# Optimization experiments

Measured on AMD Instinct MI355X. Metric: run time of the kernel, lower is better.

## Reference

```python
import jax, jax.numpy as jnp
import numpy as np

NUM_SEGMENTS = 10000
B, S, D = 4, 200000, 64

def setup_inputs() -> dict:
    key = jax.random.key(0)
    k1, k2, k3 = jax.random.split(key, 3)
    data = jax.random.normal(k1, (B, S, D), dtype=jnp.float32)
    v = jax.random.normal(k2, (B, S, D), dtype=jnp.float32)
    segment_index = jax.random.randint(k3, (S,), 0, NUM_SEGMENTS, dtype=jnp.int32)
    return {"data": data, "v": v, "segment_index": segment_index}

def reference(data, v, segment_index):
    # data participates only in the size assertion of the torch module;
    # the forward math is an unsorted segment sum of v along dim=1.
    assert data.shape == v.shape
    # out[b, s, d] = sum_{i : segment_index[i]==s} v[b, i, d]
    out = jnp.zeros((v.shape[0], NUM_SEGMENTS, v.shape[2]), dtype=v.dtype)
    out = out.at[:, segment_index, :].add(v)
    return out
```

## Files before the change

### kernel.cpp

```cpp
#include <hip/hip_runtime.h>

constexpr int NSEG = 10000;
constexpr int BB   = 4;
constexpr int SS   = 200000;
constexpr int DD   = 64;

constexpr int CAP     = 48;
constexpr int OVF_CAP = 4096;

__global__ void bucket_kernel(const int4* __restrict__ seg4,
                              int* __restrict__ cnt,
                              int* __restrict__ ovf_cnt,
                              int* __restrict__ bucket,
                              int* __restrict__ ovf) {
    int i = blockIdx.x * blockDim.x + threadIdx.x;
    if (i >= SS / 4) return;
    int4 sg = seg4[i];
    int base = i * 4;
    int ss[4] = {sg.x, sg.y, sg.z, sg.w};
    #pragma unroll
    for (int k = 0; k < 4; ++k) {
        int s = ss[k];
        int p = atomicAdd(&cnt[s], 1);
        if (p < CAP) {
            bucket[s * CAP + p] = base + k;
        } else {
            int o = atomicAdd(ovf_cnt, 1);
            if (o < OVF_CAP) ovf[o] = base + k;
        }
    }
}

__global__ void __launch_bounds__(256)
gather_kernel(const float4* __restrict__ v4,
              const int* __restrict__ cnt,
              const int* __restrict__ bucket,
              float4* __restrict__ out4) {
    int idx = blockIdx.x * blockDim.x + threadIdx.x;
    const int d4 = idx & 15;
    const int s  = idx >> 4;
    if (s >= NSEG) return;

    int n = cnt[s];
    if (n > CAP) n = CAP;
    const int* bk = bucket + s * CAP;

    float4 acc[BB];
    #pragma unroll
    for (int b = 0; b < BB; ++b) acc[b] = make_float4(0.f, 0.f, 0.f, 0.f);

    int j = 0;
    for (; j + 3 < n; j += 4) {
        int4 r = *(const int4*)(bk + j);
        #pragma unroll
        for (int b = 0; b < BB; ++b) {
            const float4* vb = v4 + (size_t)b * SS * 16;
            float4 a0 = vb[(size_t)r.x * 16 + d4];
            float4 a1 = vb[(size_t)r.y * 16 + d4];
            float4 a2 = vb[(size_t)r.z * 16 + d4];
            float4 a3 = vb[(size_t)r.w * 16 + d4];
            acc[b].x += (a0.x + a1.x) + (a2.x + a3.x);
            acc[b].y += (a0.y + a1.y) + (a2.y + a3.y);
            acc[b].z += (a0.z + a1.z) + (a2.z + a3.z);
            acc[b].w += (a0.w + a1.w) + (a2.w + a3.w);
        }
    }
    for (; j < n; ++j) {
        int r0 = bk[j];
        #pragma unroll
        for (int b = 0; b < BB; ++b) {
            float4 a0 = v4[((size_t)b * SS + r0) * 16 + d4];
            acc[b].x += a0.x; acc[b].y += a0.y;
            acc[b].z += a0.z; acc[b].w += a0.w;
        }
    }
    #pragma unroll
    for (int b = 0; b < BB; ++b)
        out4[((size_t)b * NSEG + s) * 16 + d4] = acc[b];
}

__global__ void fixup_kernel(const float4* __restrict__ v4,
                             const int* __restrict__ seg,
                             const int* __restrict__ ovf_cnt,
                             const int* __restrict__ ovf,
                             float* __restrict__ out) {
    int n = *ovf_cnt;
    if (n > OVF_CAP) n = OVF_CAP;
    for (int idx = blockIdx.x * blockDim.x + threadIdx.x; idx < n * 16;
         idx += gridDim.x * blockDim.x) {
        int r  = ovf[idx >> 4];
        int d4 = idx & 15;
        int s  = seg[r];
        #pragma unroll
        for (int b = 0; b < BB; ++b) {
            float4 a = v4[((size_t)b * SS + r) * 16 + d4];
            float* o = out + ((size_t)b * NSEG + s) * DD + d4 * 4;
            atomicAdd(o + 0, a.x);
            atomicAdd(o + 1, a.y);
            atomicAdd(o + 2, a.z);
            atomicAdd(o + 3, a.w);
        }
    }
}

__global__ void scatter_atomic_kernel(const float4* __restrict__ v4,
                                      const int* __restrict__ seg,
                                      float* __restrict__ out) {
    const int total  = BB * SS * (DD / 4);
    const int stride = gridDim.x * blockDim.x;
    for (int idx = blockIdx.x * blockDim.x + threadIdx.x; idx < total; idx += stride) {
        const int d4 = idx & 15;
        const int t  = idx >> 4;
        const int i  = t % SS;
        const int b  = t / SS;
        const int sg = seg[i];
        const float4 val = v4[idx];
        float* o = out + ((size_t)b * NSEG + sg) * DD + d4 * 4;
        atomicAdd(o + 0, val.x);
        atomicAdd(o + 1, val.y);
        atomicAdd(o + 2, val.z);
        atomicAdd(o + 3, val.w);
    }
}

extern "C" void kernel_launch(void* const* d_in, const int* in_sizes, int n_in,
                              void* d_out, int out_size, void* d_ws, size_t ws_size,
                              hipStream_t stream) {
    const float4* v4  = (const float4*)d_in[1];
    const int*    seg = (const int*)d_in[2];

    const size_t need = (size_t)(NSEG + 1 + NSEG * CAP + OVF_CAP) * sizeof(int);
    if (ws_size < need) {
        float* out = (float*)d_out;
        hipMemsetAsync(out, 0, (size_t)out_size * sizeof(float), stream);
        scatter_atomic_kernel<<<4096, 256, 0, stream>>>(v4, seg, out);
        return;
    }

    int* cnt     = (int*)d_ws;
    int* ovf_cnt = cnt + NSEG;
    int* bucket  = ovf_cnt + 1;
    int* ovf     = bucket + NSEG * CAP;

    hipMemsetAsync(cnt, 0, (size_t)(NSEG + 1) * sizeof(int), stream);

    bucket_kernel<<<(SS / 4 + 255) / 256, 256, 0, stream>>>(
        (const int4*)seg, cnt, ovf_cnt, bucket, ovf);

    const int total = NSEG * (DD / 4);
    gather_kernel<<<(total + 255) / 256, 256, 0, stream>>>(
        v4, cnt, bucket, (float4*)d_out);

    fixup_kernel<<<4, 256, 0, stream>>>(v4, seg, ovf_cnt, ovf, (float*)d_out);

    (void)in_sizes; (void)n_in; (void)out_size;
}
```

Measured before the change: 66.80 us.

## Spread batch dimension across lanes in gather and fold overflow fixup into it

The gather kernel now assigns one wave of 64 lanes per segment, with the batch index taken from the lane, so each thread accumulates a single float4 instead of four. This raises thread-level parallelism and cuts per-thread registers. The inner loop is unrolled to 8 indices for more loads in flight. The separate atomic fixup kernel is removed: each thread scans the overflow list and adds matching rows itself, saving a launch but costing a serial scan whenever overflow is non-empty.

```diff
diff --git a/kernel.cpp b/kernel.cpp
--- a/kernel.cpp
+++ b/kernel.cpp
@@ -35,72 +35,71 @@
 gather_kernel(const float4* __restrict__ v4,
               const int* __restrict__ cnt,
               const int* __restrict__ bucket,
+              const int* __restrict__ seg,
+              const int* __restrict__ ovf_cnt,
+              const int* __restrict__ ovf,
               float4* __restrict__ out4) {
-    int idx = blockIdx.x * blockDim.x + threadIdx.x;
-    const int d4 = idx & 15;
-    const int s  = idx >> 4;
+    const int idx  = blockIdx.x * blockDim.x + threadIdx.x;
+    const int lane = threadIdx.x & 63;
+    const int d4   = lane & 15;
+    const int b    = lane >> 4;
+    const int s    = idx >> 6;
     if (s >= NSEG) return;
 
     int n = cnt[s];
     if (n > CAP) n = CAP;
     const int* bk = bucket + s * CAP;
+    const float4* vb = v4 + (size_t)b * SS * 16;
 
-    float4 acc[BB];
-    #pragma unroll
-    for (int b = 0; b < BB; ++b) acc[b] = make_float4(0.f, 0.f, 0.f, 0.f);
+    float4 acc = make_float4(0.f, 0.f, 0.f, 0.f);
 
     int j = 0;
+    for (; j + 7 < n; j += 8) {
+        int4 r0 = *(const int4*)(bk + j);
+        int4 r1 = *(const int4*)(bk + j + 4);
+        float4 a0 = vb[(size_t)r0.x * 16 + d4];
+        float4 a1 = vb[(size_t)r0.y * 16 + d4];
+        float4 a2 = vb[(size_t)r0.z * 16 + d4];
+        float4 a3 = vb[(size_t)r0.w * 16 + d4];
+        float4 a4 = vb[(size_t)r1.x * 16 + d4];
+        float4 a5 = vb[(size_t)r1.y * 16 + d4];
+        float4 a6 = vb[(size_t)r1.z * 16 + d4];
+        float4 a7 = vb[(size_t)r1.w * 16 + d4];
+        acc.x += ((a0.x + a1.x) + (a2.x + a3.x)) + ((a4.x + a5.x) + (a6.x + a7.x));
+        acc.y += ((a0.y + a1.y) + (a2.y + a3.y)) + ((a4.y + a5.y) + (a6.y + a7.y));
+        acc.z += ((a0.z + a1.z) + (a2.z + a3.z)) + ((a4.z + a5.z) + (a6.z + a7.z));
+        acc.w += ((a0.w + a1.w) + (a2.w + a3.w)) + ((a4.w + a5.w) + (a6.w + a7.w));
+    }
     for (; j + 3 < n; j += 4) {
-        int4 r = *(const int4*)(bk + j);
-        #pragma unroll
-        for (int b = 0; b < BB; ++b) {
-            const float4* vb = v4 + (size_t)b * SS * 16;
-            float4 a0 = vb[(size_t)r.x * 16 + d4];
-            float4 a1 = vb[(size_t)r.y * 16 + d4];
-            float4 a2 = vb[(size_t)r.z * 16 + d4];
-            float4 a3 = vb[(size_t)r.w * 16 + d4];
-            acc[b].x += (a0.x + a1.x) + (a2.x + a3.x);
-            acc[b].y += (a0.y + a1.y) + (a2.y + a3.y);
-            acc[b].z += (a0.z + a1.z) + (a2.z + a3.z);
-            acc[b].w += (a0.w + a1.w) + (a2.w + a3.w);
-        }
+        int4 r0 = *(const int4*)(bk + j);
+        float4 a0 = vb[(size_t)r0.x * 16 + d4];
+        float4 a1 = vb[(size_t)r0.y * 16 + d4];
+        float4 a2 = vb[(size_t)r0.z * 16 + d4];
+        float4 a3 = vb[(size_t)r0.w * 16 + d4];
+        acc.x += (a0.x + a1.x) + (a2.x + a3.x);
+        acc.y += (a0.y + a1.y) + (a2.y + a3.y);
+        acc.z += (a0.z + a1.z) + (a2.z + a3.z);
+        acc.w += (a0.w + a1.w) + (a2.w + a3.w);
     }
     for (; j < n; ++j) {
         int r0 = bk[j];
-        #pragma unroll
-        for (int b = 0; b < BB; ++b) {
-            float4 a0 = v4[((size_t)b * SS + r0) * 16 + d4];
-            acc[b].x += a0.x; acc[b].y += a0.y;
-            acc[b].z += a0.z; acc[b].w += a0.w;
+        float4 a0 = vb[(size_t)r0 * 16 + d4];
+        acc.x += a0.x; acc.y += a0.y; acc.z += a0.z; acc.w += a0.w;
+    }
+
+    int no = *ovf_cnt;
+    if (no > 0) {
+        if (no > OVF_CAP) no = OVF_CAP;
+        for (int t = 0; t < no; ++t) {
+            int r = ovf[t];
+            if (seg[r] == s) {
+                float4 a0 = vb[(size_t)r * 16 + d4];
+                acc.x += a0.x; acc.y += a0.y; acc.z += a0.z; acc.w += a0.w;
+            }
         }
     }
-    #pragma unroll
-    for (int b = 0; b < BB; ++b)
-        out4[((size_t)b * NSEG + s) * 16 + d4] = acc[b];
-}
 
-__global__ void fixup_kernel(const float4* __restrict__ v4,
-                             const int* __restrict__ seg,
-                             const int* __restrict__ ovf_cnt,
-                             const int* __restrict__ ovf,
-                             float* __restrict__ out) {
-    int n = *ovf_cnt;
-    if (n > OVF_CAP) n = OVF_CAP;
-    for (int idx = blockIdx.x * blockDim.x + threadIdx.x; idx < n * 16;
-         idx += gridDim.x * blockDim.x) {
-        int r  = ovf[idx >> 4];
-        int d4 = idx & 15;
-        int s  = seg[r];
-        #pragma unroll
-        for (int b = 0; b < BB; ++b) {
-            float4 a = v4[((size_t)b * SS + r) * 16 + d4];
-            float* o = out + ((size_t)b * NSEG + s) * DD + d4 * 4;
-            atomicAdd(o + 0, a.x);
-            atomicAdd(o + 1, a.y);
-            atomicAdd(o + 2, a.z);
-            atomicAdd(o + 3, a.w);
-        }
-    }
+    out4[((size_t)b * NSEG + s) * 16 + d4] = acc;
 }
 
 __global__ void scatter_atomic_kernel(const float4* __restrict__ v4,
@@ -147,11 +146,9 @@
     bucket_kernel<<<(SS / 4 + 255) / 256, 256, 0, stream>>>(
         (const int4*)seg, cnt, ovf_cnt, bucket, ovf);
 
-    const int total = NSEG * (DD / 4);
+    const int total = NSEG * 64;
     gather_kernel<<<(total + 255) / 256, 256, 0, stream>>>(
-        v4, cnt, bucket, (float4*)d_out);
-
-    fixup_kernel<<<4, 256, 0, stream>>>(v4, seg, ovf_cnt, ovf, (float*)d_out);
+        v4, cnt, bucket, seg, ovf_cnt, ovf, (float4*)d_out);
 
     (void)in_sizes; (void)n_in; (void)out_size;
 }
```

Measured after the change: 59.90 us. 10.3% less time.
